# Performance work log

Hardware: AMD Instinct MI355X
Metric: run time of the kernel (lower is better)

The kernel has to match this reference:

```python
import jax, jax.numpy as jnp
import numpy as np

D, P, H, FF, HD = 1024, 512, 16, 4096, 64
B, L = 2, 1024
EPS = 1e-5


def rotate_half(x):
    x1, x2 = jnp.split(x, 2, axis=-1)
    return jnp.concatenate([-x2, x1], axis=-1)


def apply_rope(x, pos):  # x: [B,H,L,HD], pos: [L,HD] angles
    c = jnp.cos(pos)[None, None]
    s = jnp.sin(pos)[None, None]
    return x * c + rotate_half(x) * s


def layer_norm(x, g, b):
    mu = jnp.mean(x, axis=-1, keepdims=True)
    var = jnp.var(x, axis=-1, keepdims=True)
    return (x - mu) * jax.lax.rsqrt(var + EPS) * g + b


def heads(x):  # [B,L,D] -> [B,H,L,HD]
    Bq, Lq, _ = x.shape
    return x.reshape(Bq, Lq, H, HD).transpose(0, 2, 1, 3)


def attention(q, k, v, alibi, pos, mask):
    if pos is not None:
        q = apply_rope(q, pos)
        k = apply_rope(k, pos)
    scores = jnp.einsum('bhqd,bhkd->bhqk', q, k) * (HD ** -0.5)
    scores = jnp.where(mask[:, None, None, :], -jnp.inf, scores)
    scores = scores + alibi[None]
    w = jax.nn.softmax(scores, axis=-1)
    out = jnp.einsum('bhqk,bhkd->bhqd', w, v)
    return out.transpose(0, 2, 1, 3).reshape(out.shape[0], out.shape[2], D)


def setup_inputs() -> dict:
    key = jax.random.key(0)
    ks = iter(jax.random.split(key, 64))

    def rn(shape, scale=1.0):
        return jax.random.normal(next(ks), shape, dtype=jnp.float32) * scale

    inp = {
        'memory': rn((B, L, D)),
        'tgt': rn((B, L, D)),
        'self_alibi_bias': rn((H, L, L)),
        'self_pos_emb': rn((L, HD)),
        'cross_alibi_bias': rn((H, L, L)),
        'cross_pos_emb': rn((L, HD)),
        'mask': jax.random.randint(next(ks), (B, L), 0, 2) > 0,
        # self attention params
        'sa_lat_w': rn((D, P), 0.02), 'sa_lat_b': jnp.zeros((P,)),
        'sa_q_w': rn((P, D), 0.02), 'sa_q_b': jnp.zeros((D,)),
        'sa_k_w': rn((P, D), 0.02), 'sa_k_b': jnp.zeros((D,)),
        'sa_v_w': rn((P, D), 0.02), 'sa_v_b': jnp.zeros((D,)),
        'sa_out_w': rn((D, D), 0.02), 'sa_out_b': jnp.zeros((D,)),
        # cross attention params
        'ca_lat_w': rn((D, P), 0.02), 'ca_lat_b': jnp.zeros((P,)),
        'ca_q_w': rn((D, D), 0.02), 'ca_q_b': jnp.zeros((D,)),
        'ca_k_w': rn((P, D), 0.02), 'ca_k_b': jnp.zeros((D,)),
        'ca_v_w': rn((P, D), 0.02), 'ca_v_b': jnp.zeros((D,)),
        'ca_out_w': rn((D, D), 0.02), 'ca_out_b': jnp.zeros((D,)),
        # ffn + norms
        'lin1_w': rn((D, FF), 0.02), 'lin1_b': jnp.zeros((FF,)),
        'lin2_w': rn((FF, D), 0.02), 'lin2_b': jnp.zeros((D,)),
        'n1_g': jnp.ones((D,)), 'n1_b': jnp.zeros((D,)),
        'n2_g': jnp.ones((D,)), 'n2_b': jnp.zeros((D,)),
        'n3_g': jnp.ones((D,)), 'n3_b': jnp.zeros((D,)),
    }
    return inp


def reference(memory, tgt, self_alibi_bias, self_pos_emb, cross_alibi_bias,
              cross_pos_emb, mask,
              sa_lat_w, sa_lat_b, sa_q_w, sa_q_b, sa_k_w, sa_k_b,
              sa_v_w, sa_v_b, sa_out_w, sa_out_b,
              ca_lat_w, ca_lat_b, ca_q_w, ca_q_b, ca_k_w, ca_k_b,
              ca_v_w, ca_v_b, ca_out_w, ca_out_b,
              lin1_w, lin1_b, lin2_w, lin2_b,
              n1_g, n1_b, n2_g, n2_b, n3_g, n3_b):
    # self attention (q,k,v all from latent projection of tgt)
    proj = tgt @ sa_lat_w + sa_lat_b                      # [B,L,P]
    q = heads(proj @ sa_q_w + sa_q_b)
    k = heads(proj @ sa_k_w + sa_k_b)
    v = heads(proj @ sa_v_w + sa_v_b)
    sa = attention(q, k, v, self_alibi_bias, self_pos_emb, mask)
    sa = sa @ sa_out_w + sa_out_b
    x = tgt + layer_norm(sa, n1_g, n1_b)

    # cross attention (q from current tgt stream, k/v from latent of memory)
    mproj = memory @ ca_lat_w + ca_lat_b                  # [B,L,P]
    q = heads(x @ ca_q_w + ca_q_b)
    k = heads(mproj @ ca_k_w + ca_k_b)
    v = heads(mproj @ ca_v_w + ca_v_b)
    ca = attention(q, k, v, cross_alibi_bias, cross_pos_emb, mask)
    ca = ca @ ca_out_w + ca_out_b
    x = x + layer_norm(ca, n2_g, n2_b)

    # FFN
    f = jax.nn.gelu(x @ lin1_w + lin1_b, approximate=False) @ lin2_w + lin2_b
    x = layer_norm(x + f, n3_g, n3_b)
    return x
```

## Files before the change

### kernel.cpp

```cpp
#include <hip/hip_runtime.h>
#include <hip/hip_bf16.h>
#include <math.h>

typedef __hip_bfloat16 hbf16;
typedef __attribute__((ext_vector_type(8))) short bf16x8;
typedef __attribute__((ext_vector_type(4))) float f32x4;

constexpr int kD  = 1024;
constexpr int kP  = 512;
constexpr int kH  = 16;
constexpr int kFF = 4096;
constexpr int kHD = 64;
constexpr int kB  = 2;
constexpr int kL  = 1024;
constexpr int kTok = kB * kL;

__device__ inline short f2bf(float x) { hbf16 h = __float2bfloat16(x); return *(short*)&h; }

__device__ __forceinline__ void gload16(const void* g, void* l) {
    __builtin_amdgcn_global_load_lds(
        (const __attribute__((address_space(1))) void*)g,
        (__attribute__((address_space(3))) void*)l, 16, 0, 0);
}

__global__ __launch_bounds__(256) void cast_bf16(
    const float* __restrict__ in, short* __restrict__ out, int total4)
{
    int i = blockIdx.x * 256 + threadIdx.x;
    if (i >= total4) return;
    float4 v = *(const float4*)&in[(size_t)i * 4];
    *(short4*)&out[(size_t)i * 4] = make_short4(f2bf(v.x), f2bf(v.y), f2bf(v.z), f2bf(v.w));
}

__global__ __launch_bounds__(256) void transpose_bf16(
    const float* __restrict__ src, short* __restrict__ dst, int K, int N)
{
    __shared__ float t[32][33];
    int n0 = blockIdx.x * 32, k0 = blockIdx.y * 32;
    int tx = threadIdx.x & 31, ty = threadIdx.x >> 5;
    #pragma unroll
    for (int r = ty; r < 32; r += 8)
        t[r][tx] = src[(size_t)(k0 + r) * N + n0 + tx];
    __syncthreads();
    #pragma unroll
    for (int r = ty; r < 32; r += 8)
        dst[(size_t)(n0 + r) * K + k0 + tx] = f2bf(t[tx][r]);
}

__global__ __launch_bounds__(256) void bias_fill(
    const float* __restrict__ bias, float* __restrict__ C, int N, int total4)
{
    int i = blockIdx.x * 256 + threadIdx.x;
    if (i >= total4) return;
    int n = (i * 4) & (N - 1);
    *(float4*)&C[(size_t)i * 4] = *(const float4*)&bias[n];
}

__global__ void concat_bias(float* __restrict__ o, const float* __restrict__ a,
                            const float* __restrict__ b, const float* __restrict__ c, int n)
{
    int i = blockIdx.x * blockDim.x + threadIdx.x;
    if (i < n) o[i] = a[i];
    else if (i < 2 * n) { if (b) o[i] = b[i - n]; }
    else if (i < 3 * n) { if (c) o[i] = c[i - 2 * n]; }
}

__global__ __launch_bounds__(256) void gemm_mfma(
    const short* __restrict__ A, const short* __restrict__ WT,
    const float* __restrict__ bias, float* __restrict__ C, short* __restrict__ C16,
    int M, int N, int K, int act, int ksplit)
{
    __shared__ short As[4][4096];
    __shared__ short Bs[4][4096];
    const int tid = threadIdx.x;

    const int gx = gridDim.x;
    const int nwg = gx * gridDim.y;
    const int orig = blockIdx.y * gx + blockIdx.x;
    const int qq = nwg >> 3, rr = nwg & 7;
    const int xcd = orig & 7, lid = orig >> 3;
    const int swz = (xcd < rr) ? (xcd * (qq + 1) + lid)
                               : (rr * (qq + 1) + (xcd - rr) * qq + lid);
    const int m0 = (swz / gx) * 128, n0 = (swz % gx) * 128;

    const int ks = K / ksplit;
    const int kbeg = blockIdx.z * ks;
    const int nt = ks / 32;
    const int wave = tid >> 6, lane = tid & 63;
    const int l15 = lane & 15, quad = lane >> 4;
    const int wm = (wave & 1) * 64, wn = (wave >> 1) * 64;

    const int sgr = lane & 15;
    const int sgq = (lane >> 4) * 8;
    const size_t arow0 = (size_t)(m0 + wave * 32 + sgr) * K + sgq + kbeg;
    const size_t arow1 = arow0 + (size_t)16 * K;
    const size_t brow0 = (size_t)(n0 + wave * 32 + sgr) * K + sgq + kbeg;
    const size_t brow1 = brow0 + (size_t)16 * K;

    f32x4 acc[4][4];
    #pragma unroll
    for (int i = 0; i < 4; ++i)
        #pragma unroll
        for (int j = 0; j < 4; ++j)
            acc[i][j] = (f32x4){0.f, 0.f, 0.f, 0.f};

    auto issue = [&](int t) {
        int bi = t & 3;
        int koff = t * 32;
        gload16(&A [arow0 + koff], &As[bi][(wave * 2) * 512]);
        gload16(&A [arow1 + koff], &As[bi][(wave * 2 + 1) * 512]);
        gload16(&WT[brow0 + koff], &Bs[bi][(wave * 2) * 512]);
        gload16(&WT[brow1 + koff], &Bs[bi][(wave * 2 + 1) * 512]);
    };

    issue(0); issue(1); issue(2); issue(3);

    const int ga = (wave & 1) * 4, gb = (wave >> 1) * 4;
    for (int t = 0; t < nt; ++t) {
        int ahead = nt - 1 - t; if (ahead > 3) ahead = 3;
        if (ahead == 3)      asm volatile("s_waitcnt vmcnt(12)" ::: "memory");
        else if (ahead == 2) asm volatile("s_waitcnt vmcnt(8)"  ::: "memory");
        else if (ahead == 1) asm volatile("s_waitcnt vmcnt(4)"  ::: "memory");
        else                 asm volatile("s_waitcnt vmcnt(0)"  ::: "memory");
        __builtin_amdgcn_sched_barrier(0);
        __builtin_amdgcn_s_barrier();

        int bi = t & 3;
        bf16x8 af[4], bfr[4];
        #pragma unroll
        for (int i = 0; i < 4; ++i)
            af[i] = *(bf16x8*)&As[bi][(ga + i) * 512 + lane * 8];
        #pragma unroll
        for (int j = 0; j < 4; ++j)
            bfr[j] = *(bf16x8*)&Bs[bi][(gb + j) * 512 + lane * 8];
        #pragma unroll
        for (int i = 0; i < 4; ++i)
            #pragma unroll
            for (int j = 0; j < 4; ++j)
                acc[i][j] = __builtin_amdgcn_mfma_f32_16x16x32_bf16(af[i], bfr[j], acc[i][j], 0, 0, 0);

        asm volatile("s_waitcnt lgkmcnt(0)" ::: "memory");
        __builtin_amdgcn_sched_barrier(0);
        __builtin_amdgcn_s_barrier();
        if (t + 4 < nt) issue(t + 4);
    }

    #pragma unroll
    for (int j = 0; j < 4; ++j) {
        int n = n0 + wn + j * 16 + l15;
        if (ksplit == 1) {
            float bv = bias[n];
            #pragma unroll
            for (int i = 0; i < 4; ++i) {
                int mb = m0 + wm + i * 16 + quad * 4;
                #pragma unroll
                for (int r = 0; r < 4; ++r) {
                    float v = acc[i][j][r] + bv;
                    if (act) v = v * 0.5f * (1.0f + erff(v * 0.70710678118654752f));
                    if (C)   C[(size_t)(mb + r) * N + n] = v;
                    if (C16) C16[(size_t)(mb + r) * N + n] = f2bf(v);
                }
            }
        } else {
            #pragma unroll
            for (int i = 0; i < 4; ++i) {
                int mb = m0 + wm + i * 16 + quad * 4;
                #pragma unroll
                for (int r = 0; r < 4; ++r)
                    atomicAdd(&C[(size_t)(mb + r) * N + n], acc[i][j][r]);
            }
        }
    }
}

__global__ void qk_pack(const float* __restrict__ x, const float* __restrict__ pos,
                        short* __restrict__ outp, float scale, int ldx, int off)
{
    int idx = blockIdx.x * blockDim.x + threadIdx.x;
    if (idx >= kTok * kH * 32) return;
    int d = idx & 31;
    int h = (idx >> 5) & (kH - 1);
    int row = idx >> 9;
    int l = row & (kL - 1);
    int b = row >> 10;
    float a1 = pos[l * kHD + d];
    float a2 = pos[l * kHD + d + 32];
    size_t base = (size_t)row * ldx + off + h * kHD;
    float x1 = x[base + d], x2 = x[base + d + 32];
    float r1 = (x1 * cosf(a1) - x2 * sinf(a1)) * scale;
    float r2 = (x2 * cosf(a2) + x1 * sinf(a2)) * scale;
    size_t ob = ((size_t)(b * kH + h) * kL + l) * 64;
    outp[ob + d]      = f2bf(r1);
    outp[ob + d + 32] = f2bf(r2);
}

__global__ __launch_bounds__(256) void v_pack(const float* __restrict__ v, short* __restrict__ outp,
                                              int ldx, int off)
{
    int l0 = blockIdx.x * 64, h = blockIdx.y, b = blockIdx.z;
    __shared__ float t[64][65];
    int tid = threadIdx.x;
    #pragma unroll
    for (int e = 0; e < 4; ++e) {
        int idx = tid + e * 256;
        int r = idx >> 4, c4 = (idx & 15) * 4;
        const float4 vv = *(const float4*)&v[(size_t)(b * kL + l0 + r) * ldx + off + h * kHD + c4];
        t[r][c4] = vv.x; t[r][c4 + 1] = vv.y; t[r][c4 + 2] = vv.z; t[r][c4 + 3] = vv.w;
    }
    __syncthreads();
    int hd = tid >> 2, seg = (tid & 3) * 16;
    size_t ob = ((size_t)(b * kH + h) * 64 + hd) * kL + l0 + seg;
    short tmp[16];
    #pragma unroll
    for (int i = 0; i < 16; ++i) tmp[i] = f2bf(t[seg + i][hd]);
    #pragma unroll
    for (int i = 0; i < 16; i += 4)
        *(short4*)&outp[ob + i] = make_short4(tmp[i], tmp[i + 1], tmp[i + 2], tmp[i + 3]);
}

constexpr int AQ = 64, AK = 64;
__global__ __launch_bounds__(256, 2) void attn_mfma(
    const short* __restrict__ qpk, const short* __restrict__ kpk,
    const short* __restrict__ vpk, const float* __restrict__ alibi,
    const int* __restrict__ mask, short* __restrict__ out)
{
    const int q0 = blockIdx.x * AQ, h = blockIdx.y, b = blockIdx.z;
    const int tid = threadIdx.x, wave = tid >> 6, lane = tid & 63;
    const int l15 = lane & 15, quad = lane >> 4;
    __shared__ short Qf[4096];
    __shared__ short Kf[4096];
    __shared__ short Vf[4096];
    __shared__ float ALPS[4 * 1088];

    const short* qbase = qpk + ((size_t)(b * kH + h) * kL) * 64;
    const short* kbase = kpk + ((size_t)(b * kH + h) * kL) * 64;
    const short* vbase = vpk + ((size_t)(b * kH + h) * 64) * kL;
    const float* abase = alibi + ((size_t)h * kL + q0) * kL;
    const int*   mbase = mask + b * kL;

    const int sr = tid >> 3, sc8 = (tid & 7) * 8;
    const int sQuad = (sc8 >> 3) & 3, sS = sc8 >> 5;
    const int ar = tid >> 4, ac4 = (tid & 15) * 4;

    #pragma unroll
    for (int e = 0; e < 2; ++e) {
        int r = sr + e * 32;
        int slot = ((r >> 4) * 2 + sS) * 512 + (r & 15) * 32 + sQuad * 8;
        *(bf16x8*)&Qf[slot] = *(const bf16x8*)&qbase[(size_t)(q0 + r) * 64 + sc8];
    }

    bf16x8 rk[2], rv[2];
    float4 ral[4];
    int4 rmk;
    auto load_tile = [&](int k0) {
        #pragma unroll
        for (int e = 0; e < 2; ++e) {
            int r = sr + e * 32;
            rk[e] = *(const bf16x8*)&kbase[(size_t)(k0 + r) * 64 + sc8];
            rv[e] = *(const bf16x8*)&vbase[(size_t)r * kL + k0 + sc8];
        }
        #pragma unroll
        for (int e = 0; e < 4; ++e)
            ral[e] = *(const float4*)&abase[(size_t)(ar + e * 16) * kL + k0 + ac4];
        rmk = *(const int4*)&mbase[k0 + ac4];
    };
    auto store_tile = [&]() {
        #pragma unroll
        for (int e = 0; e < 2; ++e) {
            int r = sr + e * 32;
            int slot = ((r >> 4) * 2 + sS) * 512 + (r & 15) * 32 + sQuad * 8;
            *(bf16x8*)&Kf[slot] = rk[e];
            *(bf16x8*)&Vf[slot] = rv[e];
        }
        #pragma unroll
        for (int e = 0; e < 4; ++e) {
            float4 a = ral[e];
            a.x = rmk.x ? -1e30f : a.x;
            a.y = rmk.y ? -1e30f : a.y;
            a.z = rmk.z ? -1e30f : a.z;
            a.w = rmk.w ? -1e30f : a.w;
            *(float4*)&ALPS[(ar + e * 16) * 68 + ac4] = a;
        }
    };

    float mst[4], lst[4];
    #pragma unroll
    for (int r = 0; r < 4; ++r) { mst[r] = -3e38f; lst[r] = 0.f; }
    f32x4 oacc[4];
    #pragma unroll
    for (int j = 0; j < 4; ++j) oacc[j] = (f32x4){0.f, 0.f, 0.f, 0.f};

    load_tile(0);
    __syncthreads();

    bf16x8 aq[2];
    #pragma unroll
    for (int s = 0; s < 2; ++s)
        aq[s] = *(bf16x8*)&Qf[(wave * 2 + s) * 512 + l15 * 32 + quad * 8];

    for (int t = 0; t < kL / AK; ++t) {
        store_tile();
        __syncthreads();
        if (t + 1 < kL / AK) load_tile((t + 1) * AK);

        f32x4 sacc[4];
        #pragma unroll
        for (int nt = 0; nt < 4; ++nt) sacc[nt] = (f32x4){0.f, 0.f, 0.f, 0.f};
        #pragma unroll
        for (int nt = 0; nt < 4; ++nt)
            #pragma unroll
            for (int s = 0; s < 2; ++s) {
                bf16x8 bk = *(bf16x8*)&Kf[(nt * 2 + s) * 512 + l15 * 32 + quad * 8];
                sacc[nt] = __builtin_amdgcn_mfma_f32_16x16x32_bf16(aq[s], bk, sacc[nt], 0, 0, 0);
            }

        float sv[4][4];
        float mx[4] = {-3e38f, -3e38f, -3e38f, -3e38f};
        #pragma unroll
        for (int nt = 0; nt < 4; ++nt)
            #pragma unroll
            for (int r = 0; r < 4; ++r) {
                float al = ALPS[(wave * 16 + quad * 4 + r) * 68 + nt * 16 + l15];
                float s = sacc[nt][r] + al;
                sv[nt][r] = s;
                mx[r] = fmaxf(mx[r], s);
            }
        #pragma unroll
        for (int m = 1; m <= 8; m <<= 1)
            #pragma unroll
            for (int r = 0; r < 4; ++r)
                mx[r] = fmaxf(mx[r], __shfl_xor(mx[r], m));
        float alpha[4], lsum[4];
        #pragma unroll
        for (int r = 0; r < 4; ++r) {
            float mn = fmaxf(mst[r], mx[r]);
            alpha[r] = __expf(mst[r] - mn);
            mst[r] = mn;
            lsum[r] = 0.f;
        }
        #pragma unroll
        for (int nt = 0; nt < 4; ++nt)
            #pragma unroll
            for (int r = 0; r < 4; ++r) {
                float p = __expf(sv[nt][r] - mst[r]);
                sv[nt][r] = p;
                lsum[r] += p;
            }
        #pragma unroll
        for (int m = 1; m <= 8; m <<= 1)
            #pragma unroll
            for (int r = 0; r < 4; ++r)
                lsum[r] += __shfl_xor(lsum[r], m);
        #pragma unroll
        for (int r = 0; r < 4; ++r) lst[r] = lst[r] * alpha[r] + lsum[r];

        #pragma unroll
        for (int nt = 0; nt < 4; ++nt)
            #pragma unroll
            for (int r = 0; r < 4; ++r)
                ALPS[wave * 1088 + (quad * 4 + r) * 67 + nt * 16 + l15] = sv[nt][r];
        #pragma unroll
        for (int j = 0; j < 4; ++j)
            #pragma unroll
            for (int r = 0; r < 4; ++r)
                oacc[j][r] *= alpha[r];

        #pragma unroll
        for (int s = 0; s < 2; ++s) {
            int pb = wave * 1088 + l15 * 67 + s * 32 + quad * 8;
            bf16x8 ap;
            #pragma unroll
            for (int e = 0; e < 8; ++e) ap[e] = f2bf(ALPS[pb + e]);
            #pragma unroll
            for (int j = 0; j < 4; ++j) {
                bf16x8 bv = *(bf16x8*)&Vf[(j * 2 + s) * 512 + l15 * 32 + quad * 8];
                oacc[j] = __builtin_amdgcn_mfma_f32_16x16x32_bf16(ap, bv, oacc[j], 0, 0, 0);
            }
        }
        __syncthreads();
    }

    #pragma unroll
    for (int j = 0; j < 4; ++j)
        #pragma unroll
        for (int r = 0; r < 4; ++r) {
            int qrow = q0 + wave * 16 + quad * 4 + r;
            out[(size_t)(b * kL + qrow) * kD + h * kHD + j * 16 + l15] = f2bf(oacc[j][r] / lst[r]);
        }
}

__global__ __launch_bounds__(256) void add_ln(
    const float* __restrict__ res, const float* __restrict__ z,
    const float* __restrict__ g, const float* __restrict__ bi,
    float* __restrict__ out, short* __restrict__ out16)
{
    int row = blockIdx.x, tid = threadIdx.x;
    __shared__ float red[256], red2[256];
    const float* zr = z + (size_t)row * kD;
    float s = 0.f, sq = 0.f;
    for (int i = tid; i < kD; i += 256) { float vv = zr[i]; s += vv; sq += vv * vv; }
    red[tid] = s; red2[tid] = sq; __syncthreads();
    for (int st = 128; st > 0; st >>= 1) {
        if (tid < st) { red[tid] += red[tid + st]; red2[tid] += red2[tid + st]; }
        __syncthreads();
    }
    float mean = red[0] / kD;
    float var = red2[0] / kD - mean * mean;
    float rstd = rsqrtf(var + 1e-5f);
    for (int i = tid; i < kD; i += 256) {
        float vv = (zr[i] - mean) * rstd * g[i] + bi[i];
        float o = res[(size_t)row * kD + i] + vv;
        out[(size_t)row * kD + i] = o;
        out16[(size_t)row * kD + i] = f2bf(o);
    }
}

__global__ __launch_bounds__(256) void ln_final(
    const float* __restrict__ res, const float* __restrict__ f,
    const float* __restrict__ g, const float* __restrict__ bi,
    float* __restrict__ out)
{
    int row = blockIdx.x, tid = threadIdx.x;
    __shared__ float tt[kD];
    __shared__ float red[256], red2[256];
    float s = 0.f, sq = 0.f;
    for (int i = tid; i < kD; i += 256) {
        float vv = res[(size_t)row * kD + i] + f[(size_t)row * kD + i];
        tt[i] = vv; s += vv; sq += vv * vv;
    }
    red[tid] = s; red2[tid] = sq; __syncthreads();
    for (int st = 128; st > 0; st >>= 1) {
        if (tid < st) { red[tid] += red[tid + st]; red2[tid] += red2[tid + st]; }
        __syncthreads();
    }
    float mean = red[0] / kD;
    float var = red2[0] / kD - mean * mean;
    float rstd = rsqrtf(var + 1e-5f);
    for (int i = tid; i < kD; i += 256)
        out[(size_t)row * kD + i] = (tt[i] - mean) * rstd * g[i] + bi[i];
}

extern "C" void kernel_launch(void* const* d_in, const int* in_sizes, int n_in,
                              void* d_out, int out_size, void* d_ws, size_t ws_size,
                              hipStream_t stream)
{
    const float* memory      = (const float*)d_in[0];
    const float* tgt         = (const float*)d_in[1];
    const float* self_alibi  = (const float*)d_in[2];
    const float* self_pos    = (const float*)d_in[3];
    const float* cross_alibi = (const float*)d_in[4];
    const float* cross_pos   = (const float*)d_in[5];
    const int*   mask        = (const int*)d_in[6];
    const float* sa_lat_w = (const float*)d_in[7];   const float* sa_lat_b = (const float*)d_in[8];
    const float* sa_q_w   = (const float*)d_in[9];   const float* sa_q_b   = (const float*)d_in[10];
    const float* sa_k_w   = (const float*)d_in[11];  const float* sa_k_b   = (const float*)d_in[12];
    const float* sa_v_w   = (const float*)d_in[13];  const float* sa_v_b   = (const float*)d_in[14];
    const float* sa_out_w = (const float*)d_in[15];  const float* sa_out_b = (const float*)d_in[16];
    const float* ca_lat_w = (const float*)d_in[17];  const float* ca_lat_b = (const float*)d_in[18];
    const float* ca_q_w   = (const float*)d_in[19];  const float* ca_q_b   = (const float*)d_in[20];
    const float* ca_k_w   = (const float*)d_in[21];  const float* ca_k_b   = (const float*)d_in[22];
    const float* ca_v_w   = (const float*)d_in[23];  const float* ca_v_b   = (const float*)d_in[24];
    const float* ca_out_w = (const float*)d_in[25];  const float* ca_out_b = (const float*)d_in[26];
    const float* lin1_w   = (const float*)d_in[27];  const float* lin1_b   = (const float*)d_in[28];
    const float* lin2_w   = (const float*)d_in[29];  const float* lin2_b   = (const float*)d_in[30];
    const float* n1_g = (const float*)d_in[31];  const float* n1_b = (const float*)d_in[32];
    const float* n2_g = (const float*)d_in[33];  const float* n2_b = (const float*)d_in[34];
    const float* n3_g = (const float*)d_in[35];  const float* n3_b = (const float*)d_in[36];

    const size_t M1 = 1u << 20;
    float* W      = (float*)d_ws;
    float* xb     = W;
    short* tgt16  = (short*)W;
    float* tmp    = W + 2 * M1;
    short* mem16  = (short*)(W + 2 * M1);
    short* xb16   = (short*)(W + 4 * M1);
    float* proj   = W + 5 * M1;
    short* qpk    = (short*)(W + 5 * M1);
    short* proj16 = (short*)(W + 6 * M1);
    float* qkvb   = W + 6 * M1 + M1 / 2;
    short* attnb16= (short*)(W + 6 * M1 + M1 / 2);
    short* ffh16  = (short*)(W + 7 * M1 + M1 / 2);
    short* wslot  = (short*)(W + 12 * M1 + M1 / 2);
    short* kpk    = (short*)(W + 12 * M1 + M1 / 2);
    short* vpk    = (short*)(W + 13 * M1 + M1 / 2);
    float* bcat   = W + 14 * M1 + M1 / 2;

    auto gemm = [&](const short* A, const float* Wt, const float* bias, float* C, short* C16,
                    int M, int N, int K, int act, int S) {
        transpose_bf16<<<dim3(N / 32, K / 32), dim3(256), 0, stream>>>(Wt, wslot, K, N);
        if (S > 1)
            bias_fill<<<dim3(M * N / 1024), dim3(256), 0, stream>>>(bias, C, N, M * N / 4);
        gemm_mfma<<<dim3(N / 128, M / 128, S), dim3(256), 0, stream>>>(A, wslot, bias, C, C16, M, N, K, act, S);
    };
    dim3 agrid(kL / AQ, kH, kB);
    dim3 vgrid(kL / 64, kH, kB);
    dim3 tgD(kD / 32, kP / 32);

    cast_bf16<<<dim3(2048), dim3(256), 0, stream>>>(tgt, tgt16, kTok * kD / 4);
    gemm(tgt16, sa_lat_w, sa_lat_b, proj, nullptr, kTok, kP, kD, 0, 4);
    cast_bf16<<<dim3(1024), dim3(256), 0, stream>>>(proj, proj16, kTok * kP / 4);
    transpose_bf16<<<tgD, dim3(256), 0, stream>>>(sa_q_w, wslot, kP, kD);
    transpose_bf16<<<tgD, dim3(256), 0, stream>>>(sa_k_w, wslot + (size_t)kD * kP, kP, kD);
    transpose_bf16<<<tgD, dim3(256), 0, stream>>>(sa_v_w, wslot + (size_t)2 * kD * kP, kP, kD);
    concat_bias<<<dim3(12), dim3(256), 0, stream>>>(bcat, sa_q_b, sa_k_b, sa_v_b, kD);
    gemm_mfma<<<dim3(3 * kD / 128, kTok / 128, 1), dim3(256), 0, stream>>>(
        proj16, wslot, bcat, qkvb, nullptr, kTok, 3 * kD, kP, 0, 1);
    qk_pack<<<dim3(4096), dim3(256), 0, stream>>>(qkvb, self_pos, qpk, 0.125f, 3 * kD, 0);
    qk_pack<<<dim3(4096), dim3(256), 0, stream>>>(qkvb, self_pos, kpk, 1.0f, 3 * kD, kD);
    v_pack<<<vgrid, dim3(256), 0, stream>>>(qkvb, vpk, 3 * kD, 2 * kD);
    attn_mfma<<<agrid, dim3(256), 0, stream>>>(qpk, kpk, vpk, self_alibi, mask, attnb16);
    gemm(attnb16, sa_out_w, sa_out_b, tmp, nullptr, kTok, kD, kD, 0, 2);
    add_ln<<<dim3(kTok), dim3(256), 0, stream>>>(tgt, tmp, n1_g, n1_b, xb, xb16);

    cast_bf16<<<dim3(2048), dim3(256), 0, stream>>>(memory, mem16, kTok * kD / 4);
    gemm(mem16, ca_lat_w, ca_lat_b, proj, nullptr, kTok, kP, kD, 0, 4);
    cast_bf16<<<dim3(1024), dim3(256), 0, stream>>>(proj, proj16, kTok * kP / 4);
    float* qb  = qkvb;
    float* kvb = qkvb + 2 * M1;
    gemm(xb16, ca_q_w, ca_q_b, qb, nullptr, kTok, kD, kD, 0, 2);
    transpose_bf16<<<tgD, dim3(256), 0, stream>>>(ca_k_w, wslot, kP, kD);
    transpose_bf16<<<tgD, dim3(256), 0, stream>>>(ca_v_w, wslot + (size_t)kD * kP, kP, kD);
    concat_bias<<<dim3(8), dim3(256), 0, stream>>>(bcat, ca_k_b, ca_v_b, nullptr, kD);
    gemm_mfma<<<dim3(2 * kD / 128, kTok / 128, 1), dim3(256), 0, stream>>>(
        proj16, wslot, bcat, kvb, nullptr, kTok, 2 * kD, kP, 0, 1);
    qk_pack<<<dim3(4096), dim3(256), 0, stream>>>(qb, cross_pos, qpk, 0.125f, kD, 0);
    qk_pack<<<dim3(4096), dim3(256), 0, stream>>>(kvb, cross_pos, kpk, 1.0f, 2 * kD, 0);
    v_pack<<<vgrid, dim3(256), 0, stream>>>(kvb, vpk, 2 * kD, kD);
    attn_mfma<<<agrid, dim3(256), 0, stream>>>(qpk, kpk, vpk, cross_alibi, mask, attnb16);
    gemm(attnb16, ca_out_w, ca_out_b, tmp, nullptr, kTok, kD, kD, 0, 2);
    add_ln<<<dim3(kTok), dim3(256), 0, stream>>>(xb, tmp, n2_g, n2_b, xb, xb16);

    gemm(xb16, lin1_w, lin1_b, nullptr, ffh16, kTok, kFF, kD, 1, 1);
    gemm(ffh16, lin2_w, lin2_b, tmp, nullptr, kTok, kD, kFF, 0, 4);
    ln_final<<<dim3(kTok), dim3(256), 0, stream>>>(xb, tmp, n3_g, n3_b, (float*)d_out);
}
```

Measured before the change: 710.2 us.

## Replace split-K atomics with partial buffers reduced in fused consumer kernels

Split-K GEMMs now write each K-slice's partial sums into separate buffers instead of using atomicAdd on a bias-prefilled output. The partials, plus bias, are summed inside the downstream kernels: a reduce-and-cast kernel for the latent projections, the LayerNorm kernels, and the RoPE packing for the cross-attention query. This removes the bias_fill launches, the atomic contention and several cast passes. In exchange it uses more workspace and more memory traffic to read the partials, and the FFN second GEMM drops from a 4-way to a 2-way K split.

Measured after the change: 661.1 us. 6.9% less time.

```diff
diff --git a/kernel.cpp b/kernel.cpp
--- a/kernel.cpp
+++ b/kernel.cpp
@@ -47,15 +47,6 @@
         dst[(size_t)(n0 + r) * K + k0 + tx] = f2bf(t[tx][r]);
 }
 
-__global__ __launch_bounds__(256) void bias_fill(
-    const float* __restrict__ bias, float* __restrict__ C, int N, int total4)
-{
-    int i = blockIdx.x * 256 + threadIdx.x;
-    if (i >= total4) return;
-    int n = (i * 4) & (N - 1);
-    *(float4*)&C[(size_t)i * 4] = *(const float4*)&bias[n];
-}
-
 __global__ void concat_bias(float* __restrict__ o, const float* __restrict__ a,
                             const float* __restrict__ b, const float* __restrict__ c, int n)
 {
@@ -63,6 +54,82 @@
     if (i < n) o[i] = a[i];
     else if (i < 2 * n) { if (b) o[i] = b[i - n]; }
     else if (i < 3 * n) { if (c) o[i] = c[i - 2 * n]; }
+}
+
+__global__ __launch_bounds__(256) void reduce4_cast(
+    const float* __restrict__ p, size_t stride, const float* __restrict__ bias,
+    short* __restrict__ out16, int total4, int N)
+{
+    int i = blockIdx.x * 256 + threadIdx.x;
+    if (i >= total4) return;
+    size_t off = (size_t)i * 4;
+    int n = (int)(off & (size_t)(N - 1));
+    float4 a0 = *(const float4*)&p[off];
+    float4 a1 = *(const float4*)&p[off + stride];
+    float4 a2 = *(const float4*)&p[off + 2 * stride];
+    float4 a3 = *(const float4*)&p[off + 3 * stride];
+    float4 b  = *(const float4*)&bias[n];
+    *(short4*)&out16[off] = make_short4(
+        f2bf(a0.x + a1.x + a2.x + a3.x + b.x),
+        f2bf(a0.y + a1.y + a2.y + a3.y + b.y),
+        f2bf(a0.z + a1.z + a2.z + a3.z + b.z),
+        f2bf(a0.w + a1.w + a2.w + a3.w + b.w));
+}
+
+__global__ __launch_bounds__(256) void add_ln2(
+    const float* __restrict__ res, const float* __restrict__ p, size_t stride,
+    const float* __restrict__ bias, const float* __restrict__ g, const float* __restrict__ bi,
+    float* __restrict__ out, short* __restrict__ out16)
+{
+    int row = blockIdx.x, tid = threadIdx.x;
+    __shared__ float tt[kD];
+    __shared__ float red[256], red2[256];
+    const float* zr = p + (size_t)row * kD;
+    float s = 0.f, sq = 0.f;
+    for (int i = tid; i < kD; i += 256) {
+        float vv = zr[i] + zr[i + stride] + bias[i];
+        tt[i] = vv; s += vv; sq += vv * vv;
+    }
+    red[tid] = s; red2[tid] = sq; __syncthreads();
+    for (int st = 128; st > 0; st >>= 1) {
+        if (tid < st) { red[tid] += red[tid + st]; red2[tid] += red2[tid + st]; }
+        __syncthreads();
+    }
+    float mean = red[0] / kD;
+    float var = red2[0] / kD - mean * mean;
+    float rstd = rsqrtf(var + 1e-5f);
+    for (int i = tid; i < kD; i += 256) {
+        float vv = (tt[i] - mean) * rstd * g[i] + bi[i];
+        float o = res[(size_t)row * kD + i] + vv;
+        out[(size_t)row * kD + i] = o;
+        out16[(size_t)row * kD + i] = f2bf(o);
+    }
+}
+
+__global__ __launch_bounds__(256) void ln_final2(
+    const float* __restrict__ res, const float* __restrict__ p, size_t stride,
+    const float* __restrict__ bias, const float* __restrict__ g, const float* __restrict__ bi,
+    float* __restrict__ out)
+{
+    int row = blockIdx.x, tid = threadIdx.x;
+    __shared__ float tt[kD];
+    __shared__ float red[256], red2[256];
+    const float* zr = p + (size_t)row * kD;
+    float s = 0.f, sq = 0.f;
+    for (int i = tid; i < kD; i += 256) {
+        float vv = res[(size_t)row * kD + i] + zr[i] + zr[i + stride] + bias[i];
+        tt[i] = vv; s += vv; sq += vv * vv;
+    }
+    red[tid] = s; red2[tid] = sq; __syncthreads();
+    for (int st = 128; st > 0; st >>= 1) {
+        if (tid < st) { red[tid] += red[tid + st]; red2[tid] += red2[tid + st]; }
+        __syncthreads();
+    }
+    float mean = red[0] / kD;
+    float var = red2[0] / kD - mean * mean;
+    float rstd = rsqrtf(var + 1e-5f);
+    for (int i = tid; i < kD; i += 256)
+        out[(size_t)row * kD + i] = (tt[i] - mean) * rstd * g[i] + bi[i];
 }
 
 __global__ __launch_bounds__(256) void gemm_mfma(
@@ -145,10 +212,10 @@
         if (t + 4 < nt) issue(t + 4);
     }
 
-    #pragma unroll
-    for (int j = 0; j < 4; ++j) {
-        int n = n0 + wn + j * 16 + l15;
-        if (ksplit == 1) {
+    if (ksplit == 1) {
+        #pragma unroll
+        for (int j = 0; j < 4; ++j) {
+            int n = n0 + wn + j * 16 + l15;
             float bv = bias[n];
             #pragma unroll
             for (int i = 0; i < 4; ++i) {
@@ -161,19 +228,25 @@
                     if (C16) C16[(size_t)(mb + r) * N + n] = f2bf(v);
                 }
             }
-        } else {
+        }
+    } else {
+        float* Cp = C + (size_t)blockIdx.z * M * N;
+        #pragma unroll
+        for (int j = 0; j < 4; ++j) {
+            int n = n0 + wn + j * 16 + l15;
             #pragma unroll
             for (int i = 0; i < 4; ++i) {
                 int mb = m0 + wm + i * 16 + quad * 4;
                 #pragma unroll
                 for (int r = 0; r < 4; ++r)
-                    atomicAdd(&C[(size_t)(mb + r) * N + n], acc[i][j][r]);
+                    Cp[(size_t)(mb + r) * N + n] = acc[i][j][r];
             }
         }
     }
 }
 
-__global__ void qk_pack(const float* __restrict__ x, const float* __restrict__ pos,
+__global__ void qk_pack(const float* __restrict__ x, const float* __restrict__ x2,
+                        const float* __restrict__ qb, const float* __restrict__ pos,
                         short* __restrict__ outp, float scale, int ldx, int off)
 {
     int idx = blockIdx.x * blockDim.x + threadIdx.x;
@@ -186,9 +259,11 @@
     float a1 = pos[l * kHD + d];
     float a2 = pos[l * kHD + d + 32];
     size_t base = (size_t)row * ldx + off + h * kHD;
-    float x1 = x[base + d], x2 = x[base + d + 32];
-    float r1 = (x1 * cosf(a1) - x2 * sinf(a1)) * scale;
-    float r2 = (x2 * cosf(a2) + x1 * sinf(a2)) * scale;
+    float x1 = x[base + d], xx2 = x[base + d + 32];
+    if (x2) { x1 += x2[base + d]; xx2 += x2[base + d + 32]; }
+    if (qb) { x1 += qb[h * kHD + d]; xx2 += qb[h * kHD + d + 32]; }
+    float r1 = (x1 * cosf(a1) - xx2 * sinf(a1)) * scale;
+    float r2 = (xx2 * cosf(a2) + x1 * sinf(a2)) * scale;
     size_t ob = ((size_t)(b * kH + h) * kL + l) * 64;
     outp[ob + d]      = f2bf(r1);
     outp[ob + d + 32] = f2bf(r2);
@@ -387,57 +462,6 @@
             int qrow = q0 + wave * 16 + quad * 4 + r;
             out[(size_t)(b * kL + qrow) * kD + h * kHD + j * 16 + l15] = f2bf(oacc[j][r] / lst[r]);
         }
-}
-
-__global__ __launch_bounds__(256) void add_ln(
-    const float* __restrict__ res, const float* __restrict__ z,
-    const float* __restrict__ g, const float* __restrict__ bi,
-    float* __restrict__ out, short* __restrict__ out16)
-{
-    int row = blockIdx.x, tid = threadIdx.x;
-    __shared__ float red[256], red2[256];
-    const float* zr = z + (size_t)row * kD;
-    float s = 0.f, sq = 0.f;
-    for (int i = tid; i < kD; i += 256) { float vv = zr[i]; s += vv; sq += vv * vv; }
-    red[tid] = s; red2[tid] = sq; __syncthreads();
-    for (int st = 128; st > 0; st >>= 1) {
-        if (tid < st) { red[tid] += red[tid + st]; red2[tid] += red2[tid + st]; }
-        __syncthreads();
-    }
-    float mean = red[0] / kD;
-    float var = red2[0] / kD - mean * mean;
-    float rstd = rsqrtf(var + 1e-5f);
-    for (int i = tid; i < kD; i += 256) {
-        float vv = (zr[i] - mean) * rstd * g[i] + bi[i];
-        float o = res[(size_t)row * kD + i] + vv;
-        out[(size_t)row * kD + i] = o;
-        out16[(size_t)row * kD + i] = f2bf(o);
-    }
-}
-
-__global__ __launch_bounds__(256) void ln_final(
-    const float* __restrict__ res, const float* __restrict__ f,
-    const float* __restrict__ g, const float* __restrict__ bi,
-    float* __restrict__ out)
-{
-    int row = blockIdx.x, tid = threadIdx.x;
-    __shared__ float tt[kD];
-    __shared__ float red[256], red2[256];
-    float s = 0.f, sq = 0.f;
-    for (int i = tid; i < kD; i += 256) {
-        float vv = res[(size_t)row * kD + i] + f[(size_t)row * kD + i];
-        tt[i] = vv; s += vv; sq += vv * vv;
-    }
-    red[tid] = s; red2[tid] = sq; __syncthreads();
-    for (int st = 128; st > 0; st >>= 1) {
-        if (tid < st) { red[tid] += red[tid + st]; red2[tid] += red2[tid + st]; }
-        __syncthreads();
-    }
-    float mean = red[0] / kD;
-    float var = red2[0] / kD - mean * mean;
-    float rstd = rsqrtf(var + 1e-5f);
-    for (int i = tid; i < kD; i += 256)
-        out[(size_t)row * kD + i] = (tt[i] - mean) * rstd * g[i] + bi[i];
 }
 
 extern "C" void kernel_launch(void* const* d_in, const int* in_sizes, int n_in,
@@ -471,15 +495,16 @@
     float* W      = (float*)d_ws;
     float* xb     = W;
     short* tgt16  = (short*)W;
-    float* tmp    = W + 2 * M1;
     short* mem16  = (short*)(W + 2 * M1);
+    float* PL     = W + 2 * M1;
     short* xb16   = (short*)(W + 4 * M1);
-    float* proj   = W + 5 * M1;
     short* qpk    = (short*)(W + 5 * M1);
     short* proj16 = (short*)(W + 6 * M1);
     float* qkvb   = W + 6 * M1 + M1 / 2;
     short* attnb16= (short*)(W + 6 * M1 + M1 / 2);
     short* ffh16  = (short*)(W + 7 * M1 + M1 / 2);
+    float* PP     = W + 8 * M1 + M1 / 2;
+    float* kvb    = W + 8 * M1 + M1 / 2;
     short* wslot  = (short*)(W + 12 * M1 + M1 / 2);
     short* kpk    = (short*)(W + 12 * M1 + M1 / 2);
     short* vpk    = (short*)(W + 13 * M1 + M1 / 2);
@@ -488,49 +513,47 @@
     auto gemm = [&](const short* A, const float* Wt, const float* bias, float* C, short* C16,
                     int M, int N, int K, int act, int S) {
         transpose_bf16<<<dim3(N / 32, K / 32), dim3(256), 0, stream>>>(Wt, wslot, K, N);
-        if (S > 1)
-            bias_fill<<<dim3(M * N / 1024), dim3(256), 0, stream>>>(bias, C, N, M * N / 4);
         gemm_mfma<<<dim3(N / 128, M / 128, S), dim3(256), 0, stream>>>(A, wslot, bias, C, C16, M, N, K, act, S);
     };
     dim3 agrid(kL / AQ, kH, kB);
     dim3 vgrid(kL / 64, kH, kB);
     dim3 tgD(kD / 32, kP / 32);
+    const size_t strD = (size_t)kTok * kD;
+    const size_t strP = (size_t)kTok * kP;
 
     cast_bf16<<<dim3(2048), dim3(256), 0, stream>>>(tgt, tgt16, kTok * kD / 4);
-    gemm(tgt16, sa_lat_w, sa_lat_b, proj, nullptr, kTok, kP, kD, 0, 4);
-    cast_bf16<<<dim3(1024), dim3(256), 0, stream>>>(proj, proj16, kTok * kP / 4);
+    gemm(tgt16, sa_lat_w, sa_lat_b, PP, nullptr, kTok, kP, kD, 0, 4);
+    reduce4_cast<<<dim3(1024), dim3(256), 0, stream>>>(PP, strP, sa_lat_b, proj16, kTok * kP / 4, kP);
     transpose_bf16<<<tgD, dim3(256), 0, stream>>>(sa_q_w, wslot, kP, kD);
     transpose_bf16<<<tgD, dim3(256), 0, stream>>>(sa_k_w, wslot + (size_t)kD * kP, kP, kD);
     transpose_bf16<<<tgD, dim3(256), 0, stream>>>(sa_v_w, wslot + (size_t)2 * kD * kP, kP, kD);
     concat_bias<<<dim3(12), dim3(256), 0, stream>>>(bcat, sa_q_b, sa_k_b, sa_v_b, kD);
     gemm_mfma<<<dim3(3 * kD / 128, kTok / 128, 1), dim3(256), 0, stream>>>(
         proj16, wslot, bcat, qkvb, nullptr, kTok, 3 * kD, kP, 0, 1);
-    qk_pack<<<dim3(4096), dim3(256), 0, stream>>>(qkvb, self_pos, qpk, 0.125f, 3 * kD, 0);
-    qk_pack<<<dim3(4096), dim3(256), 0, stream>>>(qkvb, self_pos, kpk, 1.0f, 3 * kD, kD);
+    qk_pack<<<dim3(4096), dim3(256), 0, stream>>>(qkvb, nullptr, nullptr, self_pos, qpk, 0.125f, 3 * kD, 0);
+    qk_pack<<<dim3(4096), dim3(256), 0, stream>>>(qkvb, nullptr, nullptr, self_pos, kpk, 1.0f, 3 * kD, kD);
     v_pack<<<vgrid, dim3(256), 0, stream>>>(qkvb, vpk, 3 * kD, 2 * kD);
     attn_mfma<<<agrid, dim3(256), 0, stream>>>(qpk, kpk, vpk, self_alibi, mask, attnb16);
-    gemm(attnb16, sa_out_w, sa_out_b, tmp, nullptr, kTok, kD, kD, 0, 2);
-    add_ln<<<dim3(kTok), dim3(256), 0, stream>>>(tgt, tmp, n1_g, n1_b, xb, xb16);
+    gemm(attnb16, sa_out_w, sa_out_b, PP, nullptr, kTok, kD, kD, 0, 2);
+    add_ln2<<<dim3(kTok), dim3(256), 0, stream>>>(tgt, PP, strD, sa_out_b, n1_g, n1_b, xb, xb16);
 
     cast_bf16<<<dim3(2048), dim3(256), 0, stream>>>(memory, mem16, kTok * kD / 4);
-    gemm(mem16, ca_lat_w, ca_lat_b, proj, nullptr, kTok, kP, kD, 0, 4);
-    cast_bf16<<<dim3(1024), dim3(256), 0, stream>>>(proj, proj16, kTok * kP / 4);
-    float* qb  = qkvb;
-    float* kvb = qkvb + 2 * M1;
-    gemm(xb16, ca_q_w, ca_q_b, qb, nullptr, kTok, kD, kD, 0, 2);
+    gemm(mem16, ca_lat_w, ca_lat_b, PP, nullptr, kTok, kP, kD, 0, 4);
+    reduce4_cast<<<dim3(1024), dim3(256), 0, stream>>>(PP, strP, ca_lat_b, proj16, kTok * kP / 4, kP);
+    gemm(xb16, ca_q_w, ca_q_b, PP, nullptr, kTok, kD, kD, 0, 2);
+    qk_pack<<<dim3(4096), dim3(256), 0, stream>>>(PP, PP + strD, ca_q_b, cross_pos, qpk, 0.125f, kD, 0);
     transpose_bf16<<<tgD, dim3(256), 0, stream>>>(ca_k_w, wslot, kP, kD);
     transpose_bf16<<<tgD, dim3(256), 0, stream>>>(ca_v_w, wslot + (size_t)kD * kP, kP, kD);
     concat_bias<<<dim3(8), dim3(256), 0, stream>>>(bcat, ca_k_b, ca_v_b, nullptr, kD);
     gemm_mfma<<<dim3(2 * kD / 128, kTok / 128, 1), dim3(256), 0, stream>>>(
         proj16, wslot, bcat, kvb, nullptr, kTok, 2 * kD, kP, 0, 1);
-    qk_pack<<<dim3(4096), dim3(256), 0, stream>>>(qb, cross_pos, qpk, 0.125f, kD, 0);
-    qk_pack<<<dim3(4096), dim3(256), 0, stream>>>(kvb, cross_pos, kpk, 1.0f, 2 * kD, 0);
+    qk_pack<<<dim3(4096), dim3(256), 0, stream>>>(kvb, nullptr, nullptr, cross_pos, kpk, 1.0f, 2 * kD, 0);
     v_pack<<<vgrid, dim3(256), 0, stream>>>(kvb, vpk, 2 * kD, kD);
     attn_mfma<<<agrid, dim3(256), 0, stream>>>(qpk, kpk, vpk, cross_alibi, mask, attnb16);
-    gemm(attnb16, ca_out_w, ca_out_b, tmp, nullptr, kTok, kD, kD, 0, 2);
-    add_ln<<<dim3(kTok), dim3(256), 0, stream>>>(xb, tmp, n2_g, n2_b, xb, xb16);
+    gemm(attnb16, ca_out_w, ca_out_b, PP, nullptr, kTok, kD, kD, 0, 2);
+    add_ln2<<<dim3(kTok), dim3(256), 0, stream>>>(xb, PP, strD, ca_out_b, n2_g, n2_b, xb, xb16);
 
     gemm(xb16, lin1_w, lin1_b, nullptr, ffh16, kTok, kFF, kD, 1, 1);
-    gemm(ffh16, lin2_w, lin2_b, tmp, nullptr, kTok, kD, kFF, 0, 4);
-    ln_final<<<dim3(kTok), dim3(256), 0, stream>>>(xb, tmp, n3_g, n3_b, (float*)d_out);
-}
+    gemm(ffh16, lin2_w, lin2_b, PL, nullptr, kTok, kD, kFF, 0, 2);
+    ln_final2<<<dim3(kTok), dim3(256), 0, stream>>>(xb, PL, strD, lin2_b, n3_g, n3_b, (float*)d_out);
+}
```
